# Kernel optimization log

Hardware: AMD Instinct MI355X
Metric: run time of the kernel (lower is better)

Reference implementation:

```python
import jax, jax.numpy as jnp
import numpy as np

N, H, W, C = 4, 64, 64, 256
G, K = 8, 3
GC = C // G
P = K * K
PAD = 1
BN_EPS = 1e-3  # ultralytics Conv uses BatchNorm2d(eps=0.001)


def setup_inputs() -> dict:
    key = jax.random.key(0)
    ks = jax.random.split(key, 8)
    return {
        "x": jax.random.normal(ks[0], (N, H, W, C), jnp.float32),
        # depthwise conv weight (OIHW with I=1, feature_group_count=C)
        "dw_w": jax.random.normal(ks[1], (C, 1, K, K), jnp.float32) * 0.1,
        "bn_gamma": jnp.ones((C,), jnp.float32),
        "bn_beta": jnp.zeros((C,), jnp.float32),
        "bn_mean": jnp.zeros((C,), jnp.float32),
        "bn_var": jnp.ones((C,), jnp.float32),
        # offset/mask heads are zero-init in torch; use small random weights so
        # sampling locations are nontrivial but stay near the kernel grid
        "W_off": jax.random.normal(ks[2], (C, G * P * 2), jnp.float32) * 0.01,
        "b_off": jnp.zeros((G * P * 2,), jnp.float32),
        "W_mask": jax.random.normal(ks[3], (C, G * P), jnp.float32) * 0.01,
        "b_mask": jnp.zeros((G * P,), jnp.float32),
        "W_in": jax.random.normal(ks[4], (C, C), jnp.float32) / np.sqrt(C).astype(np.float32),
        "b_in": jnp.zeros((C,), jnp.float32),
        "W_out": jax.random.normal(ks[5], (C, C), jnp.float32) / np.sqrt(C).astype(np.float32),
        "b_out": jnp.zeros((C,), jnp.float32),
    }


def _grid_sample(img, grid):
    # img: (B, gc, Hi, Wi); grid: (B, L, P, 2) in [-1,1], (x,y) order.
    # Matches torch grid_sample(mode='bilinear', padding_mode='zeros', align_corners=False).
    B, gc, Hi, Wi = img.shape
    x = (grid[..., 0] + 1.0) * (Wi * 0.5) - 0.5
    y = (grid[..., 1] + 1.0) * (Hi * 0.5) - 0.5
    x0 = jnp.floor(x).astype(jnp.int32)
    y0 = jnp.floor(y).astype(jnp.int32)
    tx = x - x0
    ty = y - y0
    flat = img.reshape(B, gc, Hi * Wi)
    L, Pp = grid.shape[1], grid.shape[2]

    def tap(xi, yi, w):
        valid = (xi >= 0) & (xi < Wi) & (yi >= 0) & (yi < Hi)
        idx = jnp.clip(yi, 0, Hi - 1) * Wi + jnp.clip(xi, 0, Wi - 1)
        v = jnp.take_along_axis(flat, idx.reshape(B, 1, L * Pp), axis=2)
        v = v.reshape(B, gc, L, Pp)
        return v * (w * valid)[:, None]

    return (tap(x0, y0, (1 - tx) * (1 - ty))
            + tap(x0 + 1, y0, tx * (1 - ty))
            + tap(x0, y0 + 1, (1 - tx) * ty)
            + tap(x0 + 1, y0 + 1, tx * ty))


def _dcnv3_core(xp, offset, mask):
    # xp: (N,H,W,C) projected input; offset: (N,H,W,G*P*2); mask: (N,H,W,G*P)
    xpad = jnp.pad(xp, ((0, 0), (PAD, PAD), (PAD, PAD), (0, 0)))
    Hi, Wi = H + 2 * PAD, W + 2 * PAD
    # reference points on the padded grid, normalized to [0,1]
    start = (K - 1) // 2 + 0.5  # dilation=1, stride=1
    ref_y = (start + jnp.arange(H, dtype=jnp.float32)) / Hi
    ref_x = (start + jnp.arange(W, dtype=jnp.float32)) / Wi
    ref = jnp.stack(jnp.broadcast_arrays(ref_x[None, :], ref_y[:, None]), -1)  # (H,W,2) (x,y)
    # kernel dilation grid; torch meshgrid('ij') over (kw,kh) -> point p = iw*K + ih
    xv = jnp.arange(K, dtype=jnp.float32) - ((K - 1) // 2)
    gx, gy = jnp.meshgrid(xv / Wi, xv / Hi, indexing='ij')
    kgrid = jnp.stack([gx, gy], -1).reshape(P, 2)  # identical per group
    off = offset.reshape(N, H, W, G, P, 2) / jnp.array([Wi, Hi], jnp.float32)
    loc = ref[None, :, :, None, None, :] + kgrid[None, None, None, None] + off  # (N,H,W,G,P,2)
    sg = 2.0 * loc - 1.0
    # regroup channels-last input to (N*G, GC, Hi, Wi); channel c = g*GC + d
    img = xpad.reshape(N, Hi * Wi, G, GC).transpose(0, 2, 3, 1).reshape(N * G, GC, Hi, Wi)
    sgrid = sg.reshape(N, H * W, G, P, 2).transpose(0, 2, 1, 3, 4).reshape(N * G, H * W, P, 2)
    samp = _grid_sample(img, sgrid)  # (N*G, GC, L, P)
    m = mask.reshape(N, H * W, G, P).transpose(0, 2, 1, 3).reshape(N * G, 1, H * W, P)
    out = (samp * m).sum(-1)  # (N*G, GC, L)
    return out.reshape(N, C, H * W).transpose(0, 2, 1).reshape(N, H, W, C)


def reference(x, dw_w, bn_gamma, bn_beta, bn_mean, bn_var, W_off, b_off,
              W_mask, b_mask, W_in, b_in, W_out, b_out):
    x_proj = x @ W_in + b_in
    # depthwise 3x3 conv + BN (eval) + SiLU (ultralytics Conv)
    xc = x.transpose(0, 3, 1, 2)
    y = jax.lax.conv_general_dilated(
        xc, dw_w, (1, 1), ((PAD, PAD), (PAD, PAD)),
        feature_group_count=C, dimension_numbers=('NCHW', 'OIHW', 'NCHW'))
    scale = bn_gamma / jnp.sqrt(bn_var + BN_EPS)
    y = (y - bn_mean[None, :, None, None]) * scale[None, :, None, None] + bn_beta[None, :, None, None]
    y = y * jax.nn.sigmoid(y)
    x1 = y.transpose(0, 2, 3, 1)  # (N,H,W,C)
    offset = x1 @ W_off + b_off
    mlog = (x1 @ W_mask + b_mask).reshape(N, H, W, G, P)
    mask = jax.nn.softmax(mlog, axis=-1).reshape(N, H, W, G * P)
    out = _dcnv3_core(x_proj, offset, mask)
    return out @ W_out + b_out
```

## Files before the change

### kernel.cpp

```cpp
#include <hip/hip_runtime.h>
#include <math.h>

#define NPIX 16384
#define CC 256
#define OFFW 144
#define MSKW 72

typedef unsigned short ushortT;
typedef __attribute__((ext_vector_type(4))) float f32x4;
typedef __attribute__((ext_vector_type(8))) __bf16 bf16x8;
typedef __attribute__((ext_vector_type(8))) unsigned short u16x8;
typedef __attribute__((ext_vector_type(4))) unsigned int u32x4;

__device__ __forceinline__ float bf2f(ushortT u) {
    union { unsigned u; float f; } x; x.u = ((unsigned)u) << 16; return x.f;
}
__device__ __forceinline__ ushortT f2bf(float f) {
    union { float f; unsigned u; } x; x.f = f;
    unsigned u = x.u;
    return (ushortT)((u + 0x7FFFu + ((u >> 16) & 1u)) >> 16);
}
__device__ __forceinline__ float bflo(unsigned u) { return __uint_as_float(u << 16); }
__device__ __forceinline__ float bfhi(unsigned u) { return __uint_as_float(u & 0xFFFF0000u); }

typedef __attribute__((address_space(3))) char lds_char;
typedef __attribute__((address_space(1))) char glb_char;
__device__ __forceinline__ void gload_lds16(const void* g, void* l) {
    __builtin_amdgcn_global_load_lds((const glb_char*)g, (lds_char*)l, 16, 0, 0);
}

__global__ __launch_bounds__(256) void k_wt(
    const float* __restrict__ W_in, const float* __restrict__ W_out,
    const float* __restrict__ W_off, const float* __restrict__ W_mask,
    const float* __restrict__ b_in, const float* __restrict__ b_out,
    const float* __restrict__ b_off, const float* __restrict__ b_mask,
    ushortT* __restrict__ Wt, float* __restrict__ biasb)
{
    const int idx = blockIdx.x * 256 + threadIdx.x;
    const int slot = idx >> 16;
    const int rem = idx & 65535;
    const int n = rem >> 8, k = rem & 255;
    float v;
    if (slot == 0)      v = W_in[k * 256 + n];
    else if (slot == 1) v = W_out[k * 256 + n];
    else {
        const int g = n >> 5, r = n & 31;
        if (r < 18)      v = W_off[k * OFFW + g * 18 + r];
        else if (r < 27) v = W_mask[k * MSKW + g * 9 + (r - 18)];
        else             v = 0.f;
    }
    Wt[idx] = f2bf(v);
    if (n == 0) {
        float b;
        if (slot == 0)      b = b_in[k];
        else if (slot == 1) b = b_out[k];
        else {
            const int g = k >> 5, r = k & 31;
            b = (r < 18) ? b_off[g * 18 + r] : (r < 27 ? b_mask[g * 9 + (r - 18)] : 0.f);
        }
        biasb[slot * 256 + k] = b;
    }
}

__global__ __launch_bounds__(512, 4) void k_fused_in(
    const float* __restrict__ x, const float* __restrict__ dw_w,
    const float* __restrict__ bn_gamma, const float* __restrict__ bn_beta,
    const float* __restrict__ bn_mean, const float* __restrict__ bn_var,
    const ushortT* __restrict__ Wt, const float* __restrict__ biasb,
    ushortT* __restrict__ xpb, ushortT* __restrict__ omb)
{
    __shared__ __align__(16) ushortT xA[32 * 256];
    __shared__ __align__(16) ushortT x1s[32 * 256];
    const int tid = threadIdx.x;
    const int b0 = blockIdx.x;
    const int lb = (b0 & 7) * 64 + (b0 >> 3);
    const int base = lb * 32;
    const int n = base >> 12, h = (base >> 6) & 63, bw0 = base & 63;

    const int lane = tid & 63, wave = tid >> 6;
    const int gemm = wave >> 2, wc = wave & 3;
    const ushortT* Bt = Wt + (gemm ? 2 * 65536 : 0);

    {
        const int c = tid & 255, half = tid >> 8;
        float wreg[9];
        #pragma unroll
        for (int k = 0; k < 9; ++k) wreg[k] = dw_w[c * 9 + k];
        const float scale = bn_gamma[c] * rsqrtf(bn_var[c] + 1e-3f);
        const float mean = bn_mean[c], beta = bn_beta[c];
        const bool hv0 = h >= 1, hv2 = h <= 62;
        const float* r0 = x + ((size_t)(n * 64 + h - 1) * 64) * 256 + c;
        const float* r1 = x + ((size_t)(n * 64 + h) * 64) * 256 + c;
        const float* r2 = x + ((size_t)(n * 64 + h + 1) * 64) * 256 + c;
        const int w0 = bw0 + half * 16;
        float a0, a1, a2, e0, e1, e2;
        if (w0 - 1 >= 0) {
            a0 = hv0 ? r0[(w0 - 1) * 256] : 0.f;
            a1 = r1[(w0 - 1) * 256];
            a2 = hv2 ? r2[(w0 - 1) * 256] : 0.f;
        } else { a0 = a1 = a2 = 0.f; }
        e0 = hv0 ? r0[w0 * 256] : 0.f;
        e1 = r1[w0 * 256];
        e2 = hv2 ? r2[w0 * 256] : 0.f;
        #pragma unroll
        for (int i = 0; i < 16; ++i) {
            const int w = w0 + i;
            float d0, d1, d2;
            if (w + 1 < 64) {
                d0 = hv0 ? r0[(w + 1) * 256] : 0.f;
                d1 = r1[(w + 1) * 256];
                d2 = hv2 ? r2[(w + 1) * 256] : 0.f;
            } else { d0 = d1 = d2 = 0.f; }
            const float accv = a0 * wreg[0] + e0 * wreg[1] + d0 * wreg[2]
                             + a1 * wreg[3] + e1 * wreg[4] + d1 * wreg[5]
                             + a2 * wreg[6] + e2 * wreg[7] + d2 * wreg[8];
            const float yv = (accv - mean) * scale + beta;
            const float s = yv / (1.f + __expf(-yv));
            const int row = half * 16 + i;
            const int sb = (row * 512 + c * 2) ^ ((row & 7) << 4);
            *(ushortT*)((char*)x1s + sb) = f2bf(s);
            *(ushortT*)((char*)xA + sb) = f2bf(e1);
            a0 = e0; a1 = e1; a2 = e2;
            e0 = d0; e1 = d1; e2 = d2;
        }
    }

    bf16x8 bbp[4];
    #pragma unroll
    for (int nn = 0; nn < 4; ++nn) {
        const int ncol = wc * 64 + nn * 16 + (lane & 15);
        bbp[nn] = *(const bf16x8*)(Bt + (size_t)ncol * 256 + (lane >> 4) * 8);
    }
    __syncthreads();

    const ushortT* As = gemm ? x1s : xA;
    const float* bias = biasb + (gemm ? 512 : 0);
    ushortT* Cout = gemm ? omb : xpb;

    f32x4 acc[2][4];
    #pragma unroll
    for (int m = 0; m < 2; ++m)
        #pragma unroll
        for (int nn = 0; nn < 4; ++nn) acc[m][nn] = (f32x4){0.f, 0.f, 0.f, 0.f};

    #pragma unroll
    for (int k0 = 0; k0 < 256; k0 += 32) {
        bf16x8 af[2], bb[4];
        #pragma unroll
        for (int nn = 0; nn < 4; ++nn) bb[nn] = bbp[nn];
        if (k0 + 32 < 256) {
            #pragma unroll
            for (int nn = 0; nn < 4; ++nn) {
                const int ncol = wc * 64 + nn * 16 + (lane & 15);
                bbp[nn] = *(const bf16x8*)(Bt + (size_t)ncol * 256 + (k0 + 32) + (lane >> 4) * 8);
            }
        }
        #pragma unroll
        for (int m = 0; m < 2; ++m) {
            const int row = m * 16 + (lane & 15);
            af[m] = *(const bf16x8*)((const char*)As + row * 512 +
                     (((k0 + (lane >> 4) * 8) * 2) ^ ((row & 7) << 4)));
        }
        #pragma unroll
        for (int m = 0; m < 2; ++m)
            #pragma unroll
            for (int nn = 0; nn < 4; ++nn)
                acc[m][nn] = __builtin_amdgcn_mfma_f32_16x16x32_bf16(af[m], bb[nn], acc[m][nn], 0, 0, 0);
    }

    const int rbase = (lane >> 4) * 4, col16 = lane & 15;
    #pragma unroll
    for (int m = 0; m < 2; ++m) {
        #pragma unroll
        for (int nn = 0; nn < 4; ++nn) {
            const int col = wc * 64 + nn * 16 + col16;
            const float bj = bias[col];
            #pragma unroll
            for (int r = 0; r < 4; ++r) {
                const int row = m * 16 + rbase + r;
                Cout[(size_t)(base + row) * 256 + col] = f2bf(acc[m][nn][r] + bj);
            }
        }
    }
}

__global__ __launch_bounds__(256) void k_core(
    const ushortT* __restrict__ omb, const ushortT* __restrict__ xpb,
    ushortT* __restrict__ coreb)
{
    __shared__ __align__(16) float wtab[8][72][8];
    const int tid = threadIdx.x;
    const int b0 = blockIdx.x;
    const int lb = (b0 & 7) * 256 + (b0 >> 3);
    const int base = lb * 8;
    const int n = base >> 12, h = (base >> 6) & 63, w0 = base & 63;

    if (tid < 64) {
        const int px = tid >> 3, g = tid & 7;
        const ushortT* omp = omb + (size_t)(base + px) * 256 + g * 32;
        const u32x4 L0 = *(const u32x4*)(omp);
        const u32x4 L1 = *(const u32x4*)(omp + 8);
        const u32x4 L2 = *(const u32x4*)(omp + 16);
        const u32x4 L3 = *(const u32x4*)(omp + 24);
        unsigned opair[9];
        #pragma unroll
        for (int p = 0; p < 4; ++p) { opair[p] = L0[p]; opair[4 + p] = L1[p]; }
        opair[8] = L2[0];
        float lg[9];
        lg[0] = bflo(L2[1]); lg[1] = bfhi(L2[1]);
        lg[2] = bflo(L2[2]); lg[3] = bfhi(L2[2]);
        lg[4] = bflo(L2[3]); lg[5] = bfhi(L2[3]);
        lg[6] = bflo(L3[0]); lg[7] = bfhi(L3[0]);
        lg[8] = bflo(L3[1]);
        float mx = -1e30f;
        #pragma unroll
        for (int p = 0; p < 9; ++p) mx = fmaxf(mx, lg[p]);
        float e[9], sum = 0.f;
        #pragma unroll
        for (int p = 0; p < 9; ++p) { e[p] = __expf(lg[p] - mx); sum += e[p]; }
        const float inv = 1.f / sum;
        #pragma unroll
        for (int p = 0; p < 9; ++p) {
            const float m = e[p] * inv;
            const float ox = bflo(opair[p]), oy = bfhi(opair[p]);
            const float pxc = (float)(w0 + px + p / 3) + ox;
            const float pyc = (float)(h + p % 3) + oy;
            const float xf = floorf(pxc), yf = floorf(pyc);
            const float tx = pxc - xf, ty = pyc - yf;
            const int x0 = (int)xf - 1, y0 = (int)yf - 1;
            const int x1 = x0 + 1, y1 = y0 + 1;
            const float wx0 = ((unsigned)x0 < 64u) ? (1.f - tx) : 0.f;
            const float wx1 = ((unsigned)x1 < 64u) ? tx : 0.f;
            const float wy0 = ((unsigned)y0 < 64u) ? (1.f - ty) : 0.f;
            const float wy1 = ((unsigned)y1 < 64u) ? ty : 0.f;
            const int cx0 = min(max(x0, 0), 63), cx1 = min(max(x1, 0), 63);
            const int cy0 = min(max(y0, 0), 63), cy1 = min(max(y1, 0), 63);
            float* dst = wtab[px][g * 9 + p];
            float4 idx4, wt4;
            idx4.x = __int_as_float((cy0 * 64 + cx0) * 256);
            idx4.y = __int_as_float((cy0 * 64 + cx1) * 256);
            idx4.z = __int_as_float((cy1 * 64 + cx0) * 256);
            idx4.w = __int_as_float((cy1 * 64 + cx1) * 256);
            wt4.x = m * wx0 * wy0; wt4.y = m * wx1 * wy0;
            wt4.z = m * wx0 * wy1; wt4.w = m * wx1 * wy1;
            *(float4*)dst = idx4;
            *(float4*)(dst + 4) = wt4;
        }
    }
    __syncthreads();

    const int px = tid >> 5, g = (tid >> 2) & 7, o = tid & 3;
    const ushortT* xn = xpb + (size_t)n * (4096 * 256) + g * 32 + o * 8;
    float acc[8];
    #pragma unroll
    for (int j = 0; j < 8; ++j) acc[j] = 0.f;
    #pragma unroll
    for (int p = 0; p < 9; ++p) {
        const float* wt = wtab[px][g * 9 + p];
        const int4 o4 = *(const int4*)(wt);
        const float4 w4 = *(const float4*)(wt + 4);
        const u32x4 A = *(const u32x4*)(xn + o4.x);
        const u32x4 B = *(const u32x4*)(xn + o4.y);
        const u32x4 C = *(const u32x4*)(xn + o4.z);
        const u32x4 D = *(const u32x4*)(xn + o4.w);
        #pragma unroll
        for (int i = 0; i < 4; ++i) {
            acc[2 * i]     += w4.x * bflo(A[i]) + w4.y * bflo(B[i])
                            + w4.z * bflo(C[i]) + w4.w * bflo(D[i]);
            acc[2 * i + 1] += w4.x * bfhi(A[i]) + w4.y * bfhi(B[i])
                            + w4.z * bfhi(C[i]) + w4.w * bfhi(D[i]);
        }
    }
    u16x8 cv;
    #pragma unroll
    for (int j = 0; j < 8; ++j) cv[j] = f2bf(acc[j]);
    *(u16x8*)(coreb + (size_t)(base + px) * 256 + g * 32 + o * 8) = cv;
}

__global__ __launch_bounds__(512) void k_gemm_out(
    const ushortT* __restrict__ A, const ushortT* __restrict__ Bt,
    const float* __restrict__ bias, float* __restrict__ out)
{
    __shared__ __align__(16) ushortT As[32 * 256];
    const int tid = threadIdx.x;
    const int m0 = blockIdx.x * 32;
    const int lane = tid & 63, wave = tid >> 6;

    #pragma unroll
    for (int it = 0; it < 2; ++it) {
        const int i = it * 512 + tid;
        const int row = i >> 5, ch = i & 31;
        const int sch = ch ^ (row & 7);
        gload_lds16(A + (size_t)(m0 + row) * 256 + sch * 8, (char*)As + i * 16);
    }
    bf16x8 bbp[2];
    #pragma unroll
    for (int nn = 0; nn < 2; ++nn) {
        const int ncol = wave * 32 + nn * 16 + (lane & 15);
        bbp[nn] = *(const bf16x8*)(Bt + (size_t)ncol * 256 + (lane >> 4) * 8);
    }
    asm volatile("s_waitcnt vmcnt(0)");
    __syncthreads();

    f32x4 acc[2][2];
    #pragma unroll
    for (int m = 0; m < 2; ++m)
        #pragma unroll
        for (int nn = 0; nn < 2; ++nn) acc[m][nn] = (f32x4){0.f, 0.f, 0.f, 0.f};

    #pragma unroll
    for (int k0 = 0; k0 < 256; k0 += 32) {
        bf16x8 af[2], bb[2];
        #pragma unroll
        for (int nn = 0; nn < 2; ++nn) bb[nn] = bbp[nn];
        if (k0 + 32 < 256) {
            #pragma unroll
            for (int nn = 0; nn < 2; ++nn) {
                const int ncol = wave * 32 + nn * 16 + (lane & 15);
                bbp[nn] = *(const bf16x8*)(Bt + (size_t)ncol * 256 + (k0 + 32) + (lane >> 4) * 8);
            }
        }
        #pragma unroll
        for (int m = 0; m < 2; ++m) {
            const int row = m * 16 + (lane & 15);
            af[m] = *(const bf16x8*)((const char*)As + row * 512 +
                     (((k0 + (lane >> 4) * 8) * 2) ^ ((row & 7) << 4)));
        }
        #pragma unroll
        for (int m = 0; m < 2; ++m)
            #pragma unroll
            for (int nn = 0; nn < 2; ++nn)
                acc[m][nn] = __builtin_amdgcn_mfma_f32_16x16x32_bf16(af[m], bb[nn], acc[m][nn], 0, 0, 0);
    }

    const int rbase = (lane >> 4) * 4, col16 = lane & 15;
    #pragma unroll
    for (int m = 0; m < 2; ++m) {
        #pragma unroll
        for (int nn = 0; nn < 2; ++nn) {
            const int col = wave * 32 + nn * 16 + col16;
            const float bj = bias[col];
            #pragma unroll
            for (int r = 0; r < 4; ++r) {
                const int row = m0 + m * 16 + rbase + r;
                out[(size_t)row * 256 + col] = acc[m][nn][r] + bj;
            }
        }
    }
}

extern "C" void kernel_launch(void* const* d_in, const int* in_sizes, int n_in,
                              void* d_out, int out_size, void* d_ws, size_t ws_size,
                              hipStream_t stream) {
    const float* x        = (const float*)d_in[0];
    const float* dw_w     = (const float*)d_in[1];
    const float* bn_gamma = (const float*)d_in[2];
    const float* bn_beta  = (const float*)d_in[3];
    const float* bn_mean  = (const float*)d_in[4];
    const float* bn_var   = (const float*)d_in[5];
    const float* W_off    = (const float*)d_in[6];
    const float* b_off    = (const float*)d_in[7];
    const float* W_mask   = (const float*)d_in[8];
    const float* b_mask   = (const float*)d_in[9];
    const float* W_in     = (const float*)d_in[10];
    const float* b_in     = (const float*)d_in[11];
    const float* W_out    = (const float*)d_in[12];
    const float* b_out    = (const float*)d_in[13];
    float* out = (float*)d_out;

    char* w = (char*)d_ws;
    ushortT* Wt    = (ushortT*)w;
    float* biasb   = (float*)(w + 393216);
    ushortT* xpb   = (ushortT*)(w + 396288);
    ushortT* omb   = (ushortT*)(w + 396288 + 8388608);
    ushortT* coreb = (ushortT*)(w + 396288 + 2 * 8388608);

    hipLaunchKernelGGL(k_wt, dim3(768), dim3(256), 0, stream,
                       W_in, W_out, W_off, W_mask, b_in, b_out, b_off, b_mask, Wt, biasb);
    hipLaunchKernelGGL(k_fused_in, dim3(512), dim3(512), 0, stream,
                       x, dw_w, bn_gamma, bn_beta, bn_mean, bn_var, Wt, biasb, xpb, omb);
    hipLaunchKernelGGL(k_core, dim3(2048), dim3(256), 0, stream,
                       omb, xpb, coreb);
    hipLaunchKernelGGL(k_gemm_out, dim3(NPIX / 32), dim3(512), 0, stream,
                       coreb, Wt + 65536, biasb + 256, out);
}
```

Before: 66.96 us.

## Recompute sampling weights per thread, widen LDS swizzle, use hardware bf16/rcp

The core kernel drops its shared-memory weight table and the barrier that followed it. Each thread now recomputes the softmax and bilinear offsets and weights for its own pixel and group, which duplicates that math across the 4 threads sharing a group. The LDS XOR swizzle in both GEMM kernels widens from 8 to 16 rows to reduce bank conflicts on MFMA fragment loads. The bf16 conversion now uses a native cast and SiLU/softmax use the hardware reciprocal, which trades some accuracy for fewer instructions.

```diff
diff --git a/kernel.cpp b/kernel.cpp
--- a/kernel.cpp
+++ b/kernel.cpp
@@ -16,9 +16,10 @@
     union { unsigned u; float f; } x; x.u = ((unsigned)u) << 16; return x.f;
 }
 __device__ __forceinline__ ushortT f2bf(float f) {
-    union { float f; unsigned u; } x; x.f = f;
-    unsigned u = x.u;
-    return (ushortT)((u + 0x7FFFu + ((u >> 16) & 1u)) >> 16);
+    __bf16 h = (__bf16)f;
+    ushortT u;
+    __builtin_memcpy(&u, &h, 2);
+    return u;
 }
 __device__ __forceinline__ float bflo(unsigned u) { return __uint_as_float(u << 16); }
 __device__ __forceinline__ float bfhi(unsigned u) { return __uint_as_float(u & 0xFFFF0000u); }
@@ -115,9 +116,9 @@
                              + a1 * wreg[3] + e1 * wreg[4] + d1 * wreg[5]
                              + a2 * wreg[6] + e2 * wreg[7] + d2 * wreg[8];
             const float yv = (accv - mean) * scale + beta;
-            const float s = yv / (1.f + __expf(-yv));
+            const float s = yv * __builtin_amdgcn_rcpf(1.f + __expf(-yv));
             const int row = half * 16 + i;
-            const int sb = (row * 512 + c * 2) ^ ((row & 7) << 4);
+            const int sb = (row * 512 + c * 2) ^ ((row & 15) << 4);
             *(ushortT*)((char*)x1s + sb) = f2bf(s);
             *(ushortT*)((char*)xA + sb) = f2bf(e1);
             a0 = e0; a1 = e1; a2 = e2;
@@ -159,7 +160,7 @@
         for (int m = 0; m < 2; ++m) {
             const int row = m * 16 + (lane & 15);
             af[m] = *(const bf16x8*)((const char*)As + row * 512 +
-                     (((k0 + (lane >> 4) * 8) * 2) ^ ((row & 7) << 4)));
+                     (((k0 + (lane >> 4) * 8) * 2) ^ ((row & 15) << 4)));
         }
         #pragma unroll
         for (int m = 0; m < 2; ++m)
@@ -188,87 +189,74 @@
     const ushortT* __restrict__ omb, const ushortT* __restrict__ xpb,
     ushortT* __restrict__ coreb)
 {
-    __shared__ __align__(16) float wtab[8][72][8];
     const int tid = threadIdx.x;
     const int b0 = blockIdx.x;
     const int lb = (b0 & 7) * 256 + (b0 >> 3);
     const int base = lb * 8;
     const int n = base >> 12, h = (base >> 6) & 63, w0 = base & 63;
 
-    if (tid < 64) {
-        const int px = tid >> 3, g = tid & 7;
-        const ushortT* omp = omb + (size_t)(base + px) * 256 + g * 32;
-        const u32x4 L0 = *(const u32x4*)(omp);
-        const u32x4 L1 = *(const u32x4*)(omp + 8);
-        const u32x4 L2 = *(const u32x4*)(omp + 16);
-        const u32x4 L3 = *(const u32x4*)(omp + 24);
-        unsigned opair[9];
-        #pragma unroll
-        for (int p = 0; p < 4; ++p) { opair[p] = L0[p]; opair[4 + p] = L1[p]; }
-        opair[8] = L2[0];
-        float lg[9];
-        lg[0] = bflo(L2[1]); lg[1] = bfhi(L2[1]);
-        lg[2] = bflo(L2[2]); lg[3] = bfhi(L2[2]);
-        lg[4] = bflo(L2[3]); lg[5] = bfhi(L2[3]);
-        lg[6] = bflo(L3[0]); lg[7] = bfhi(L3[0]);
-        lg[8] = bflo(L3[1]);
-        float mx = -1e30f;
-        #pragma unroll
-        for (int p = 0; p < 9; ++p) mx = fmaxf(mx, lg[p]);
-        float e[9], sum = 0.f;
-        #pragma unroll
-        for (int p = 0; p < 9; ++p) { e[p] = __expf(lg[p] - mx); sum += e[p]; }
-        const float inv = 1.f / sum;
-        #pragma unroll
-        for (int p = 0; p < 9; ++p) {
-            const float m = e[p] * inv;
-            const float ox = bflo(opair[p]), oy = bfhi(opair[p]);
-            const float pxc = (float)(w0 + px + p / 3) + ox;
-            const float pyc = (float)(h + p % 3) + oy;
-            const float xf = floorf(pxc), yf = floorf(pyc);
-            const float tx = pxc - xf, ty = pyc - yf;
-            const int x0 = (int)xf - 1, y0 = (int)yf - 1;
-            const int x1 = x0 + 1, y1 = y0 + 1;
-            const float wx0 = ((unsigned)x0 < 64u) ? (1.f - tx) : 0.f;
-            const float wx1 = ((unsigned)x1 < 64u) ? tx : 0.f;
-            const float wy0 = ((unsigned)y0 < 64u) ? (1.f - ty) : 0.f;
-            const float wy1 = ((unsigned)y1 < 64u) ? ty : 0.f;
-            const int cx0 = min(max(x0, 0), 63), cx1 = min(max(x1, 0), 63);
-            const int cy0 = min(max(y0, 0), 63), cy1 = min(max(y1, 0), 63);
-            float* dst = wtab[px][g * 9 + p];
-            float4 idx4, wt4;
-            idx4.x = __int_as_float((cy0 * 64 + cx0) * 256);
-            idx4.y = __int_as_float((cy0 * 64 + cx1) * 256);
-            idx4.z = __int_as_float((cy1 * 64 + cx0) * 256);
-            idx4.w = __int_as_float((cy1 * 64 + cx1) * 256);
-            wt4.x = m * wx0 * wy0; wt4.y = m * wx1 * wy0;
-            wt4.z = m * wx0 * wy1; wt4.w = m * wx1 * wy1;
-            *(float4*)dst = idx4;
-            *(float4*)(dst + 4) = wt4;
-        }
-    }
-    __syncthreads();
-
     const int px = tid >> 5, g = (tid >> 2) & 7, o = tid & 3;
+
+    const ushortT* omp = omb + (size_t)(base + px) * 256 + g * 32;
+    const u32x4 L0 = *(const u32x4*)(omp);
+    const u32x4 L1 = *(const u32x4*)(omp + 8);
+    const u32x4 L2 = *(const u32x4*)(omp + 16);
+    const u32x4 L3 = *(const u32x4*)(omp + 24);
+    unsigned opair[9];
+    #pragma unroll
+    for (int p = 0; p < 4; ++p) { opair[p] = L0[p]; opair[4 + p] = L1[p]; }
+    opair[8] = L2[0];
+    float lg[9];
+    lg[0] = bflo(L2[1]); lg[1] = bfhi(L2[1]);
+    lg[2] = bflo(L2[2]); lg[3] = bfhi(L2[2]);
+    lg[4] = bflo(L2[3]); lg[5] = bfhi(L2[3]);
+    lg[6] = bflo(L3[0]); lg[7] = bfhi(L3[0]);
+    lg[8] = bflo(L3[1]);
+    float mx = -1e30f;
+    #pragma unroll
+    for (int p = 0; p < 9; ++p) mx = fmaxf(mx, lg[p]);
+    float sum = 0.f;
+    #pragma unroll
+    for (int p = 0; p < 9; ++p) sum += __expf(lg[p] - mx);
+    const float inv = __builtin_amdgcn_rcpf(sum);
+
     const ushortT* xn = xpb + (size_t)n * (4096 * 256) + g * 32 + o * 8;
     float acc[8];
     #pragma unroll
     for (int j = 0; j < 8; ++j) acc[j] = 0.f;
+
     #pragma unroll
     for (int p = 0; p < 9; ++p) {
-        const float* wt = wtab[px][g * 9 + p];
-        const int4 o4 = *(const int4*)(wt);
-        const float4 w4 = *(const float4*)(wt + 4);
-        const u32x4 A = *(const u32x4*)(xn + o4.x);
-        const u32x4 B = *(const u32x4*)(xn + o4.y);
-        const u32x4 C = *(const u32x4*)(xn + o4.z);
-        const u32x4 D = *(const u32x4*)(xn + o4.w);
+        const float m = __expf(lg[p] - mx) * inv;
+        const float ox = bflo(opair[p]), oy = bfhi(opair[p]);
+        const float pxc = (float)(w0 + px + p / 3) + ox;
+        const float pyc = (float)(h + p % 3) + oy;
+        const float xf = floorf(pxc), yf = floorf(pyc);
+        const float tx = pxc - xf, ty = pyc - yf;
+        const int x0 = (int)xf - 1, y0 = (int)yf - 1;
+        const int x1 = x0 + 1, y1 = y0 + 1;
+        const float wx0 = ((unsigned)x0 < 64u) ? (1.f - tx) : 0.f;
+        const float wx1 = ((unsigned)x1 < 64u) ? tx : 0.f;
+        const float wy0 = ((unsigned)y0 < 64u) ? (1.f - ty) : 0.f;
+        const float wy1 = ((unsigned)y1 < 64u) ? ty : 0.f;
+        const int cx0 = min(max(x0, 0), 63), cx1 = min(max(x1, 0), 63);
+        const int cy0 = min(max(y0, 0), 63), cy1 = min(max(y1, 0), 63);
+        const int o00 = (cy0 * 64 + cx0) * 256;
+        const int o10 = (cy0 * 64 + cx1) * 256;
+        const int o01 = (cy1 * 64 + cx0) * 256;
+        const int o11 = (cy1 * 64 + cx1) * 256;
+        const float w00 = m * wx0 * wy0, w10 = m * wx1 * wy0;
+        const float w01 = m * wx0 * wy1, w11 = m * wx1 * wy1;
+        const u32x4 A = *(const u32x4*)(xn + o00);
+        const u32x4 B = *(const u32x4*)(xn + o10);
+        const u32x4 C = *(const u32x4*)(xn + o01);
+        const u32x4 D = *(const u32x4*)(xn + o11);
         #pragma unroll
         for (int i = 0; i < 4; ++i) {
-            acc[2 * i]     += w4.x * bflo(A[i]) + w4.y * bflo(B[i])
-                            + w4.z * bflo(C[i]) + w4.w * bflo(D[i]);
-            acc[2 * i + 1] += w4.x * bfhi(A[i]) + w4.y * bfhi(B[i])
-                            + w4.z * bfhi(C[i]) + w4.w * bfhi(D[i]);
+            acc[2 * i]     += w00 * bflo(A[i]) + w10 * bflo(B[i])
+                            + w01 * bflo(C[i]) + w11 * bflo(D[i]);
+            acc[2 * i + 1] += w00 * bfhi(A[i]) + w10 * bfhi(B[i])
+                            + w01 * bfhi(C[i]) + w11 * bfhi(D[i]);
         }
     }
     u16x8 cv;
@@ -290,7 +278,7 @@
     for (int it = 0; it < 2; ++it) {
         const int i = it * 512 + tid;
         const int row = i >> 5, ch = i & 31;
-        const int sch = ch ^ (row & 7);
+        const int sch = ch ^ (row & 15);
         gload_lds16(A + (size_t)(m0 + row) * 256 + sch * 8, (char*)As + i * 16);
     }
     bf16x8 bbp[2];
@@ -324,7 +312,7 @@
         for (int m = 0; m < 2; ++m) {
             const int row = m * 16 + (lane & 15);
             af[m] = *(const bf16x8*)((const char*)As + row * 512 +
-                     (((k0 + (lane >> 4) * 8) * 2) ^ ((row & 7) << 4)));
+                     (((k0 + (lane >> 4) * 8) * 2) ^ ((row & 15) << 4)));
         }
         #pragma unroll
         for (int m = 0; m < 2; ++m)
```

Measured after the change: 63.88 us. -4.6%, faster.
